# Performance work log

Measured on AMD Instinct MI355X. Metric: run time of the kernel, lower is better.

The kernel has to match this reference:

```python
import jax, jax.numpy as jnp
import numpy as np

N = 50000          # nodes
E_RAND = 800000    # random edges
E = E_RAND + N     # + self loops -> 850000
F_IN = 256         # nembed
F_HID = 64         # nhid
H = 8              # nheads
NCLASS = 40
ALPHA = 0.2        # leakyrelu slope


def setup_inputs() -> dict:
    key = jax.random.key(0)
    ks = jax.random.split(key, 8)
    x = jax.random.normal(ks[0], (N, F_IN), dtype=jnp.float32)
    # random edges + self loops (guarantees every row-sum > 0, like adj + I)
    er = jax.random.randint(ks[1], (2, E_RAND), 0, N, dtype=jnp.int32)
    loops = jnp.tile(jnp.arange(N, dtype=jnp.int32)[None, :], (2, 1))
    edge_index = jnp.concatenate([er, loops], axis=1)  # [2, E]
    # per-head attention params (xavier-ish scale)
    W = jax.random.normal(ks[2], (H, F_IN, F_HID), dtype=jnp.float32) * (1.0 / np.sqrt(F_IN))
    a = jax.random.normal(ks[3], (H, 2 * F_HID), dtype=jnp.float32) * 0.1
    Wo = jax.random.normal(ks[4], (H * F_HID, F_HID), dtype=jnp.float32) * (1.0 / np.sqrt(H * F_HID))
    ao = jax.random.normal(ks[5], (2 * F_HID,), dtype=jnp.float32) * 0.1
    mlp_w = jax.random.normal(ks[6], (NCLASS, F_HID), dtype=jnp.float32) * 0.05
    mlp_b = jnp.zeros((NCLASS,), dtype=jnp.float32)
    return {"x": x, "edge_index": edge_index, "W": W, "a": a,
            "Wo": Wo, "ao": ao, "mlp_w": mlp_w, "mlp_b": mlp_b}


def _leaky(v):
    return jnp.where(v > 0, v, ALPHA * v)


def _spgat_layer(x, W, a, src, dst, n):
    """pyGAT SpGraphAttentionLayer (eval mode, dropout = identity).
    out[i] = sum_{e: src=i} exp(-leakyrelu(a.[h_src;h_dst])) * h[dst] / rowsum_i
    """
    h = x @ W                         # [N, D]
    D = W.shape[1]
    s_src = h @ a[:D]                 # [N]
    s_dst = h @ a[D:]                 # [N]
    # per-edge unnormalized attention (note the -exp(leaky) of original sp impl)
    e = jnp.exp(-_leaky(s_src[src] + s_dst[dst]))          # [E]
    rowsum = jax.ops.segment_sum(e, src, num_segments=n)   # [N]
    num = jax.ops.segment_sum(e[:, None] * h[dst], src, num_segments=n)  # [N, D]
    return num / rowsum[:, None]


def reference(x, edge_index, W, a, Wo, ao, mlp_w, mlp_b):
    src, dst = edge_index[0], edge_index[1]
    # multi-head attention, concat=True -> elu inside each head
    heads = [jax.nn.elu(_spgat_layer(x, W[i], a[i], src, dst, N)) for i in range(H)]
    xc = jnp.concatenate(heads, axis=1)                     # [N, H*F_HID]
    # dropout (eval) = identity
    xo = jax.nn.elu(_spgat_layer(xc, Wo, ao, src, dst, N))  # [N, F_HID]
    return xo @ mlp_w.T + mlp_b                             # [N, NCLASS]
```

## Files before the change

### kernel.cpp

```cpp
#include <hip/hip_runtime.h>

#define NN 50000
#define HH 8
#define ALPHA 0.2f
#define NPAD 50048

typedef short short8 __attribute__((ext_vector_type(8)));
typedef float f32x4 __attribute__((ext_vector_type(4)));

__device__ __forceinline__ float elu_f(float x) {
  return x > 0.f ? x : __expf(x) - 1.f;
}

__device__ __forceinline__ unsigned short f2bf(float f) {
  unsigned int u = __float_as_uint(f);
  unsigned int r = (u + 0x7fffu + ((u >> 16) & 1u)) >> 16;
  return (unsigned short)r;
}

__global__ void cvt_x_kernel(const float* __restrict__ x, unsigned short* __restrict__ xb,
                             int total4) {
  int i = blockIdx.x * 256 + threadIdx.x;
  if (i >= total4) return;
  float4 v = ((const float4*)x)[i];
  ushort4 o;
  o.x = f2bf(v.x); o.y = f2bf(v.y); o.z = f2bf(v.z); o.w = f2bf(v.w);
  ((ushort4*)xb)[i] = o;
}

__global__ void cvt_w_kernel(const float* __restrict__ W, unsigned short* __restrict__ Wt,
                             int K, int total) {
  int tid = blockIdx.x * 256 + threadIdx.x;
  if (tid >= total) return;
  int h = tid / (K * 64);
  int rem = tid - h * K * 64;
  int k = rem >> 6, c = rem & 63;
  Wt[((size_t)h * 64 + c) * K + k] = f2bf(W[tid]);
}

__global__ void hist_kernel(const int* __restrict__ src, int* __restrict__ cnt, int E) {
  int e = blockIdx.x * blockDim.x + threadIdx.x;
  if (e < E) atomicAdd(&cnt[src[e]], 1);
}

__global__ __launch_bounds__(1024) void scan_blocks_kernel(const int* __restrict__ cnt,
    int* __restrict__ tmp, int* __restrict__ bsum, int n) {
  __shared__ int sh[1024];
  int i = blockIdx.x * 1024 + threadIdx.x;
  int v = (i < n) ? cnt[i] : 0;
  sh[threadIdx.x] = v;
  __syncthreads();
  for (int off = 1; off < 1024; off <<= 1) {
    int t = (threadIdx.x >= off) ? sh[threadIdx.x - off] : 0;
    __syncthreads();
    sh[threadIdx.x] += t;
    __syncthreads();
  }
  if (i < n) tmp[i] = sh[threadIdx.x] - v;
  if (threadIdx.x == 1023) bsum[blockIdx.x] = sh[1023];
}

__global__ __launch_bounds__(64) void scan_top_kernel(const int* __restrict__ bsum,
    int* __restrict__ boffs, int nb) {
  int L = threadIdx.x;
  int v = (L < nb) ? bsum[L] : 0;
  int incl = v;
#pragma unroll
  for (int off = 1; off < 64; off <<= 1) {
    int t = __shfl_up(incl, off, 64);
    if (L >= off) incl += t;
  }
  if (L < nb) boffs[L] = incl - v;
}

__global__ __launch_bounds__(1024) void scan_apply_kernel(const int* __restrict__ tmp,
    const int* __restrict__ boffs, int* __restrict__ row_ptr, int* __restrict__ nxt,
    int n, int E) {
  int i = blockIdx.x * 1024 + threadIdx.x;
  if (i < n) {
    int s = tmp[i] + boffs[blockIdx.x];
    row_ptr[i] = s;
    nxt[i] = s;
  }
  if (i == 0) row_ptr[n] = E;
}

__global__ void scatter_kernel(const int* __restrict__ src, const int* __restrict__ dst,
                               int* __restrict__ nxt, int* __restrict__ col, int E) {
  int e = blockIdx.x * blockDim.x + threadIdx.x;
  if (e < E) {
    int p = atomicAdd(&nxt[src[e]], 1);
    col[p] = dst[e];
  }
}

template <int MT>
__global__ __launch_bounds__(256) void mfma_gemm_kernel(
    const unsigned short* __restrict__ A, const unsigned short* __restrict__ Bt,
    const float* __restrict__ Aatt, unsigned short* __restrict__ Cout,
    float* __restrict__ ss, float* __restrict__ sd,
    int N, int K, int tab_stride, int score_stride) {
  extern __shared__ unsigned short Bs[];
  const int y = blockIdx.y;
  const int Kp = K + 8;

  {
    const unsigned short* Bsrc = Bt + (size_t)y * 64 * K;
    int nchunk = 64 * (K >> 3);
    for (int c = threadIdx.x; c < nchunk; c += 256) {
      int n = c / (K >> 3);
      int kq = (c - n * (K >> 3)) << 3;
      *(uint4*)&Bs[n * Kp + kq] = *(const uint4*)(Bsrc + (size_t)n * K + kq);
    }
  }
  __syncthreads();

  int w = threadIdx.x >> 6, L = threadIdx.x & 63;
  int quad = L >> 4, l16 = L & 15;
  int m0 = blockIdx.x * (64 * MT) + w * (16 * MT);

  f32x4 acc[MT][4];
#pragma unroll
  for (int mt = 0; mt < MT; ++mt)
#pragma unroll
    for (int nt = 0; nt < 4; ++nt) acc[mt][nt] = (f32x4)(0.f);

  const unsigned short* Arow[MT];
#pragma unroll
  for (int mt = 0; mt < MT; ++mt)
    Arow[mt] = A + (size_t)(m0 + mt * 16 + l16) * K + quad * 8;

  short8 a_cur[MT];
#pragma unroll
  for (int mt = 0; mt < MT; ++mt) a_cur[mt] = *(const short8*)(Arow[mt]);

  for (int k0 = 0; k0 < K; k0 += 32) {
    short8 a_nxt[MT];
    if (k0 + 32 < K) {
#pragma unroll
      for (int mt = 0; mt < MT; ++mt) a_nxt[mt] = *(const short8*)(Arow[mt] + k0 + 32);
    }
#pragma unroll
    for (int nt = 0; nt < 4; ++nt) {
      short8 b = *(const short8*)&Bs[(l16 + 16 * nt) * Kp + k0 + quad * 8];
#pragma unroll
      for (int mt = 0; mt < MT; ++mt)
        acc[mt][nt] = __builtin_amdgcn_mfma_f32_16x16x32_bf16(a_cur[mt], b, acc[mt][nt], 0, 0, 0);
    }
#pragma unroll
    for (int mt = 0; mt < MT; ++mt) a_cur[mt] = a_nxt[mt];
  }

  float as[4], ad[4];
#pragma unroll
  for (int nt = 0; nt < 4; ++nt) {
    as[nt] = Aatt[y * 128 + l16 + 16 * nt];
    ad[nt] = Aatt[y * 128 + 64 + l16 + 16 * nt];
  }
#pragma unroll
  for (int mt = 0; mt < MT; ++mt) {
#pragma unroll
    for (int reg = 0; reg < 4; ++reg) {
      float p = 0.f, q = 0.f;
#pragma unroll
      for (int nt = 0; nt < 4; ++nt) {
        p += acc[mt][nt][reg] * as[nt];
        q += acc[mt][nt][reg] * ad[nt];
      }
#pragma unroll
      for (int off = 1; off < 16; off <<= 1) {
        p += __shfl_xor(p, off, 64);
        q += __shfl_xor(q, off, 64);
      }
      int row = m0 + mt * 16 + quad * 4 + reg;
      if (l16 == 0 && row < N) {
        ss[(size_t)row * score_stride + y] = p;
        sd[(size_t)row * score_stride + y] = q;
      }
    }
#pragma unroll
    for (int reg = 0; reg < 4; ++reg) {
      int row = m0 + mt * 16 + quad * 4 + reg;
      if (row < N) {
#pragma unroll
        for (int nt = 0; nt < 4; ++nt)
          Cout[(size_t)row * tab_stride + y * 64 + l16 + 16 * nt] = f2bf(acc[mt][nt][reg]);
      }
    }
  }
}

__global__ __launch_bounds__(256) void agg1_kernel(const unsigned short* __restrict__ table,
    const float* __restrict__ ss, const float* __restrict__ sd,
    const int* __restrict__ row_ptr, const int* __restrict__ col,
    unsigned short* __restrict__ xc, int N) {
  int wid = threadIdx.x >> 6, L = threadIdx.x & 63;
  int n = blockIdx.x * 4 + wid;
  if (n >= N) return;
  int h = L >> 3;
  int b = L & 7;
  int srcsel = h << 3;
  float ssn = ss[n * 8 + h];
  int k0 = row_ptr[n], deg = row_ptr[n + 1] - k0;
  float acc[8];
#pragma unroll
  for (int t = 0; t < 8; ++t) acc[t] = 0.f;
  float rs = 0.f;

  for (int c0 = 0; c0 < deg; c0 += 64) {
    int j = c0 + L;
    int d_l = (j < deg) ? col[k0 + j] : 0;
    int m = min(64, deg - c0);
    for (int g = 0; g < m; g += 8) {
      int eoff = g + b;
      int de = __shfl(d_l, eoff, 64);
      float sv = sd[(size_t)de * 8 + h];
      float s = ssn + sv;
      float e = __expf(-fmaxf(s, ALPHA * s));
      if (eoff >= m) e = 0.f;
      rs += e;
      int gm = min(8, m - g);
      int d0 = __builtin_amdgcn_readlane(d_l, g);
      uint4 rv = *((const uint4*)(table + (size_t)d0 * 512) + L);
      for (int jj = 0; jj < gm; ++jj) {
        uint4 cur = rv;
        if (jj + 1 < gm) {
          int dn = __builtin_amdgcn_readlane(d_l, g + jj + 1);
          rv = *((const uint4*)(table + (size_t)dn * 512) + L);
        }
        float ew = __shfl(e, srcsel + jj, 64);
        const unsigned int* up = (const unsigned int*)&cur;
#pragma unroll
        for (int w = 0; w < 4; ++w) {
          acc[2 * w]     += ew * __uint_as_float(up[w] << 16);
          acc[2 * w + 1] += ew * __uint_as_float(up[w] & 0xffff0000u);
        }
      }
    }
  }
  rs += __shfl_xor(rs, 1, 64);
  rs += __shfl_xor(rs, 2, 64);
  rs += __shfl_xor(rs, 4, 64);
  float inv = 1.f / rs;
  short8 pk;
#pragma unroll
  for (int t = 0; t < 8; ++t) pk[t] = (short)f2bf(elu_f(acc[t] * inv));
  *(short8*)(xc + (size_t)n * 512 + L * 8) = pk;
}

__global__ __launch_bounds__(256) void agg2_kernel(const unsigned short* __restrict__ table,
    const float* __restrict__ ss, const float* __restrict__ sd,
    const int* __restrict__ row_ptr, const int* __restrict__ col,
    float* __restrict__ xo, int N) {
  int wid = threadIdx.x >> 6, L = threadIdx.x & 63;
  int n = blockIdx.x * 4 + wid;
  if (n >= N) return;
  float ssn = ss[n];
  int k0 = row_ptr[n], deg = row_ptr[n + 1] - k0;
  float acc = 0.f, rs = 0.f;
  const char* base = (const char*)table;

  for (int c0 = 0; c0 < deg; c0 += 64) {
    int j = c0 + L;
    int d_l = 0;
    float e_l = 0.f;
    if (j < deg) {
      d_l = col[k0 + j];
      float s = ssn + sd[d_l];
      e_l = __expf(-fmaxf(s, ALPHA * s));
    }
    rs += e_l;
    int m = min(64, deg - c0);
    int off_l = d_l << 7;
    int so = __builtin_amdgcn_readlane(off_l, 0);
    unsigned hv = *(const unsigned short*)(base + so + L * 2);
    for (int jj = 0; jj < m; ++jj) {
      unsigned cur = hv;
      if (jj + 1 < m) {
        so = __builtin_amdgcn_readlane(off_l, jj + 1);
        hv = *(const unsigned short*)(base + so + L * 2);
      }
      float ew = __uint_as_float(
          (unsigned)__builtin_amdgcn_readlane(__float_as_uint(e_l), jj));
      acc += ew * __uint_as_float(cur << 16);
    }
  }
#pragma unroll
  for (int off = 1; off < 64; off <<= 1) rs += __shfl_xor(rs, off, 64);
  xo[(size_t)n * 64 + L] = elu_f(acc / rs);
}

__global__ __launch_bounds__(256) void final_kernel(const float* __restrict__ xo,
    const float* __restrict__ mlp_w, const float* __restrict__ mlp_b,
    float* __restrict__ out, int total) {
  __shared__ float wsh[40 * 65];
  __shared__ float bsh[40];
  for (int i = threadIdx.x; i < 40 * 64; i += 256) wsh[(i >> 6) * 65 + (i & 63)] = mlp_w[i];
  if (threadIdx.x < 40) bsh[threadIdx.x] = mlp_b[threadIdx.x];
  __syncthreads();
  int idx = blockIdx.x * 256 + threadIdx.x;
  if (idx >= total) return;
  int n = idx / 40, c = idx - n * 40;
  const float* xr = xo + (size_t)n * 64;
  const float* wr = wsh + c * 65;
  float acc = bsh[c];
#pragma unroll
  for (int j = 0; j < 64; ++j) acc += xr[j] * wr[j];
  out[idx] = acc;
}

extern "C" void kernel_launch(void* const* d_in, const int* in_sizes, int n_in,
                              void* d_out, int out_size, void* d_ws, size_t ws_size,
                              hipStream_t stream) {
  (void)n_in; (void)out_size; (void)ws_size;
  const float* x  = (const float*)d_in[0];
  const int*   ei = (const int*)d_in[1];
  const float* W  = (const float*)d_in[2];
  const float* a  = (const float*)d_in[3];
  const float* Wo = (const float*)d_in[4];
  const float* ao = (const float*)d_in[5];
  const float* mw = (const float*)d_in[6];
  const float* mb = (const float*)d_in[7];
  float* out = (float*)d_out;

  const int N = NN;
  const int E = in_sizes[1] / 2;
  const int* src = ei;
  const int* dst = ei + E;

  char* ws = (char*)d_ws;
  size_t off = 0;
  auto alloc = [&](size_t bytes) {
    char* p = ws + off;
    off = (off + bytes + 255) & ~(size_t)255;
    return p;
  };
  unsigned short* xb  = (unsigned short*)alloc((size_t)NPAD * 256 * 2);
  unsigned short* Wt  = (unsigned short*)alloc((size_t)HH * 64 * 256 * 2);
  unsigned short* Wot = (unsigned short*)alloc((size_t)64 * 512 * 2);
  unsigned short* h1b = (unsigned short*)alloc((size_t)N * 512 * 2);
  float* ss1     = (float*)alloc((size_t)N * 8 * 4);
  float* sd1     = (float*)alloc((size_t)N * 8 * 4);
  unsigned short* xc = (unsigned short*)alloc((size_t)NPAD * 512 * 2);
  unsigned short* h2b = (unsigned short*)alloc((size_t)N * 64 * 2);
  float* ss2     = (float*)alloc((size_t)N * 4);
  float* sd2     = (float*)alloc((size_t)N * 4);
  float* xo      = (float*)alloc((size_t)N * 64 * 4);
  int*   row_ptr = (int*)  alloc((size_t)(N + 1) * 4);
  int*   nxt     = (int*)  alloc((size_t)N * 4);
  int*   cnt     = (int*)  alloc((size_t)N * 4);
  int*   tmp     = (int*)  alloc((size_t)N * 4);
  int*   bsum    = (int*)  alloc(64 * 4);
  int*   boffs   = (int*)  alloc(64 * 4);
  int*   colv    = (int*)  alloc((size_t)E * 4);

  int eb = (E + 255) / 256;
  int nb1024 = (N + 1023) / 1024;

  hipLaunchKernelGGL(cvt_x_kernel, dim3((N * 256 / 4 + 255) / 256), dim3(256), 0, stream,
                     x, xb, N * 256 / 4);
  hipLaunchKernelGGL(cvt_w_kernel, dim3((HH * 256 * 64 + 255) / 256), dim3(256), 0, stream,
                     W, Wt, 256, HH * 256 * 64);
  hipLaunchKernelGGL(cvt_w_kernel, dim3((512 * 64 + 255) / 256), dim3(256), 0, stream,
                     Wo, Wot, 512, 512 * 64);

  hipMemsetAsync(cnt, 0, (size_t)N * 4, stream);
  hipLaunchKernelGGL(hist_kernel, dim3(eb), dim3(256), 0, stream, src, cnt, E);
  hipLaunchKernelGGL(scan_blocks_kernel, dim3(nb1024), dim3(1024), 0, stream, cnt, tmp, bsum, N);
  hipLaunchKernelGGL(scan_top_kernel, dim3(1), dim3(64), 0, stream, bsum, boffs, nb1024);
  hipLaunchKernelGGL(scan_apply_kernel, dim3(nb1024), dim3(1024), 0, stream, tmp, boffs, row_ptr, nxt, N, E);
  hipLaunchKernelGGL(scatter_kernel, dim3(eb), dim3(256), 0, stream, src, dst, nxt, colv, E);

  hipLaunchKernelGGL((mfma_gemm_kernel<2>), dim3(NPAD / 128, HH), dim3(256),
                     64 * (256 + 8) * 2, stream,
                     xb, Wt, a, h1b, ss1, sd1, N, 256, 512, 8);
  hipLaunchKernelGGL(agg1_kernel, dim3((N + 3) / 4), dim3(256), 0, stream,
                     h1b, ss1, sd1, row_ptr, colv, xc, N);

  hipLaunchKernelGGL((mfma_gemm_kernel<1>), dim3(NPAD / 64, 1), dim3(256),
                     64 * (512 + 8) * 2, stream,
                     xc, Wot, ao, h2b, ss2, sd2, N, 512, 64, 1);
  hipLaunchKernelGGL(agg2_kernel, dim3((N + 3) / 4), dim3(256), 0, stream,
                     h2b, ss2, sd2, row_ptr, colv, xo, N);

  hipLaunchKernelGGL(final_kernel, dim3((N * 40 + 255) / 256), dim3(256), 0, stream,
                     xo, mw, mb, out, N * 40);
}
```

Baseline: 494.1 us.

## Fuse conversion kernels, restructure GEMM1 over heads, batch gather loads in aggregation

Merges the three fp32-to-bf16 conversion kernels into one launch. The first GEMM now loads each block's A rows into registers once and loops over all 8 heads, reloading B per head, instead of using a 2D grid that re-reads A for every head. Both aggregation kernels issue up to 8 independent gather loads before consuming them, replacing the one-ahead software prefetch, to raise memory-level parallelism. This costs more registers and adds per-head syncthreads in the GEMM, and the GEMM launches fewer, longer blocks.

```diff
diff --git a/kernel.cpp b/kernel.cpp
--- a/kernel.cpp
+++ b/kernel.cpp
@@ -18,24 +18,31 @@
   return (unsigned short)r;
 }
 
-__global__ void cvt_x_kernel(const float* __restrict__ x, unsigned short* __restrict__ xb,
-                             int total4) {
-  int i = blockIdx.x * 256 + threadIdx.x;
-  if (i >= total4) return;
-  float4 v = ((const float4*)x)[i];
-  ushort4 o;
-  o.x = f2bf(v.x); o.y = f2bf(v.y); o.z = f2bf(v.z); o.w = f2bf(v.w);
-  ((ushort4*)xb)[i] = o;
-}
-
-__global__ void cvt_w_kernel(const float* __restrict__ W, unsigned short* __restrict__ Wt,
-                             int K, int total) {
+__global__ void cvt_all_kernel(const float* __restrict__ x, unsigned short* __restrict__ xb,
+                               const float* __restrict__ W, unsigned short* __restrict__ Wt,
+                               const float* __restrict__ Wo, unsigned short* __restrict__ Wot,
+                               int n4x) {
   int tid = blockIdx.x * 256 + threadIdx.x;
-  if (tid >= total) return;
-  int h = tid / (K * 64);
-  int rem = tid - h * K * 64;
-  int k = rem >> 6, c = rem & 63;
-  Wt[((size_t)h * 64 + c) * K + k] = f2bf(W[tid]);
+  if (tid < n4x) {
+    float4 v = ((const float4*)x)[tid];
+    ushort4 o;
+    o.x = f2bf(v.x); o.y = f2bf(v.y); o.z = f2bf(v.z); o.w = f2bf(v.w);
+    ((ushort4*)xb)[tid] = o;
+    return;
+  }
+  int t1 = tid - n4x;
+  if (t1 < HH * 256 * 64) {
+    int h = t1 / (256 * 64);
+    int rem = t1 - h * 256 * 64;
+    int k = rem >> 6, c = rem & 63;
+    Wt[((size_t)h * 64 + c) * 256 + k] = f2bf(W[t1]);
+    return;
+  }
+  int t2 = t1 - HH * 256 * 64;
+  if (t2 < 512 * 64) {
+    int k = t2 >> 6, c = t2 & 63;
+    Wot[(size_t)c * 512 + k] = f2bf(Wo[t2]);
+  }
 }
 
 __global__ void hist_kernel(const int* __restrict__ src, int* __restrict__ cnt, int E) {
@@ -94,98 +101,147 @@
   }
 }
 
-template <int MT>
-__global__ __launch_bounds__(256) void mfma_gemm_kernel(
+__global__ __launch_bounds__(256) void mfma_gemm1_kernel(
     const unsigned short* __restrict__ A, const unsigned short* __restrict__ Bt,
     const float* __restrict__ Aatt, unsigned short* __restrict__ Cout,
-    float* __restrict__ ss, float* __restrict__ sd,
-    int N, int K, int tab_stride, int score_stride) {
-  extern __shared__ unsigned short Bs[];
-  const int y = blockIdx.y;
-  const int Kp = K + 8;
-
-  {
-    const unsigned short* Bsrc = Bt + (size_t)y * 64 * K;
-    int nchunk = 64 * (K >> 3);
-    for (int c = threadIdx.x; c < nchunk; c += 256) {
-      int n = c / (K >> 3);
-      int kq = (c - n * (K >> 3)) << 3;
-      *(uint4*)&Bs[n * Kp + kq] = *(const uint4*)(Bsrc + (size_t)n * K + kq);
-    }
-  }
-  __syncthreads();
-
+    float* __restrict__ ss, float* __restrict__ sd, int N) {
+  __shared__ unsigned short Bs[64][264];
   int w = threadIdx.x >> 6, L = threadIdx.x & 63;
   int quad = L >> 4, l16 = L & 15;
-  int m0 = blockIdx.x * (64 * MT) + w * (16 * MT);
-
-  f32x4 acc[MT][4];
-#pragma unroll
-  for (int mt = 0; mt < MT; ++mt)
-#pragma unroll
-    for (int nt = 0; nt < 4; ++nt) acc[mt][nt] = (f32x4)(0.f);
-
-  const unsigned short* Arow[MT];
-#pragma unroll
-  for (int mt = 0; mt < MT; ++mt)
-    Arow[mt] = A + (size_t)(m0 + mt * 16 + l16) * K + quad * 8;
-
-  short8 a_cur[MT];
-#pragma unroll
-  for (int mt = 0; mt < MT; ++mt) a_cur[mt] = *(const short8*)(Arow[mt]);
-
-  for (int k0 = 0; k0 < K; k0 += 32) {
-    short8 a_nxt[MT];
-    if (k0 + 32 < K) {
-#pragma unroll
-      for (int mt = 0; mt < MT; ++mt) a_nxt[mt] = *(const short8*)(Arow[mt] + k0 + 32);
-    }
+  int m0 = blockIdx.x * 64;
+  int myrow = m0 + w * 16 + l16;
+
+  const unsigned short* Ar = A + (size_t)myrow * 256 + quad * 8;
+  short8 areg[8];
+#pragma unroll
+  for (int ks = 0; ks < 8; ++ks) areg[ks] = *(const short8*)(Ar + ks * 32);
+
+  for (int y = 0; y < HH; ++y) {
+    __syncthreads();
+    {
+      const unsigned short* Bsrc = Bt + (size_t)y * 64 * 256;
+      for (int c = threadIdx.x; c < 2048; c += 256) {
+        int n = c >> 5;
+        int kq = (c & 31) << 3;
+        *(uint4*)&Bs[n][kq] = *(const uint4*)(Bsrc + (size_t)n * 256 + kq);
+      }
+    }
+    __syncthreads();
+
+    f32x4 acc[4];
+#pragma unroll
+    for (int nt = 0; nt < 4; ++nt) acc[nt] = (f32x4)(0.f);
+#pragma unroll
+    for (int ks = 0; ks < 8; ++ks) {
+#pragma unroll
+      for (int nt = 0; nt < 4; ++nt) {
+        short8 b = *(const short8*)&Bs[l16 + 16 * nt][ks * 32 + quad * 8];
+        acc[nt] = __builtin_amdgcn_mfma_f32_16x16x32_bf16(areg[ks], b, acc[nt], 0, 0, 0);
+      }
+    }
+
+    float as[4], ad[4];
 #pragma unroll
     for (int nt = 0; nt < 4; ++nt) {
-      short8 b = *(const short8*)&Bs[(l16 + 16 * nt) * Kp + k0 + quad * 8];
-#pragma unroll
-      for (int mt = 0; mt < MT; ++mt)
-        acc[mt][nt] = __builtin_amdgcn_mfma_f32_16x16x32_bf16(a_cur[mt], b, acc[mt][nt], 0, 0, 0);
-    }
-#pragma unroll
-    for (int mt = 0; mt < MT; ++mt) a_cur[mt] = a_nxt[mt];
-  }
-
-  float as[4], ad[4];
-#pragma unroll
-  for (int nt = 0; nt < 4; ++nt) {
-    as[nt] = Aatt[y * 128 + l16 + 16 * nt];
-    ad[nt] = Aatt[y * 128 + 64 + l16 + 16 * nt];
-  }
-#pragma unroll
-  for (int mt = 0; mt < MT; ++mt) {
+      as[nt] = Aatt[y * 128 + l16 + 16 * nt];
+      ad[nt] = Aatt[y * 128 + 64 + l16 + 16 * nt];
+    }
 #pragma unroll
     for (int reg = 0; reg < 4; ++reg) {
       float p = 0.f, q = 0.f;
 #pragma unroll
       for (int nt = 0; nt < 4; ++nt) {
-        p += acc[mt][nt][reg] * as[nt];
-        q += acc[mt][nt][reg] * ad[nt];
+        p += acc[nt][reg] * as[nt];
+        q += acc[nt][reg] * ad[nt];
       }
 #pragma unroll
       for (int off = 1; off < 16; off <<= 1) {
         p += __shfl_xor(p, off, 64);
         q += __shfl_xor(q, off, 64);
       }
-      int row = m0 + mt * 16 + quad * 4 + reg;
+      int row = m0 + w * 16 + quad * 4 + reg;
       if (l16 == 0 && row < N) {
-        ss[(size_t)row * score_stride + y] = p;
-        sd[(size_t)row * score_stride + y] = q;
+        ss[(size_t)row * 8 + y] = p;
+        sd[(size_t)row * 8 + y] = q;
       }
     }
 #pragma unroll
     for (int reg = 0; reg < 4; ++reg) {
-      int row = m0 + mt * 16 + quad * 4 + reg;
+      int row = m0 + w * 16 + quad * 4 + reg;
       if (row < N) {
 #pragma unroll
         for (int nt = 0; nt < 4; ++nt)
-          Cout[(size_t)row * tab_stride + y * 64 + l16 + 16 * nt] = f2bf(acc[mt][nt][reg]);
-      }
+          Cout[(size_t)row * 512 + y * 64 + l16 + 16 * nt] = f2bf(acc[nt][reg]);
+      }
+    }
+  }
+}
+
+__global__ __launch_bounds__(256) void mfma_gemm2_kernel(
+    const unsigned short* __restrict__ A, const unsigned short* __restrict__ Bt,
+    const float* __restrict__ Aatt, unsigned short* __restrict__ Cout,
+    float* __restrict__ ss, float* __restrict__ sd, int N) {
+  __shared__ unsigned short Bs[64][520];
+  {
+    for (int c = threadIdx.x; c < 4096; c += 256) {
+      int n = c >> 6;
+      int kq = (c & 63) << 3;
+      *(uint4*)&Bs[n][kq] = *(const uint4*)(Bt + (size_t)n * 512 + kq);
+    }
+  }
+  __syncthreads();
+
+  int w = threadIdx.x >> 6, L = threadIdx.x & 63;
+  int quad = L >> 4, l16 = L & 15;
+  int m0 = blockIdx.x * 64;
+  int myrow = m0 + w * 16 + l16;
+  const unsigned short* Ar = A + (size_t)myrow * 512 + quad * 8;
+
+  f32x4 acc[4];
+#pragma unroll
+  for (int nt = 0; nt < 4; ++nt) acc[nt] = (f32x4)(0.f);
+
+  short8 a_cur = *(const short8*)(Ar);
+  for (int k0 = 0; k0 < 512; k0 += 32) {
+    short8 a_nxt;
+    if (k0 + 32 < 512) a_nxt = *(const short8*)(Ar + k0 + 32);
+#pragma unroll
+    for (int nt = 0; nt < 4; ++nt) {
+      short8 b = *(const short8*)&Bs[l16 + 16 * nt][k0 + quad * 8];
+      acc[nt] = __builtin_amdgcn_mfma_f32_16x16x32_bf16(a_cur, b, acc[nt], 0, 0, 0);
+    }
+    a_cur = a_nxt;
+  }
+
+  float as[4], ad[4];
+#pragma unroll
+  for (int nt = 0; nt < 4; ++nt) {
+    as[nt] = Aatt[l16 + 16 * nt];
+    ad[nt] = Aatt[64 + l16 + 16 * nt];
+  }
+#pragma unroll
+  for (int reg = 0; reg < 4; ++reg) {
+    float p = 0.f, q = 0.f;
+#pragma unroll
+    for (int nt = 0; nt < 4; ++nt) {
+      p += acc[nt][reg] * as[nt];
+      q += acc[nt][reg] * ad[nt];
+    }
+#pragma unroll
+    for (int off = 1; off < 16; off <<= 1) {
+      p += __shfl_xor(p, off, 64);
+      q += __shfl_xor(q, off, 64);
+    }
+    int row = m0 + w * 16 + quad * 4 + reg;
+    if (l16 == 0 && row < N) { ss[row] = p; sd[row] = q; }
+  }
+#pragma unroll
+  for (int reg = 0; reg < 4; ++reg) {
+    int row = m0 + w * 16 + quad * 4 + reg;
+    if (row < N) {
+#pragma unroll
+      for (int nt = 0; nt < 4; ++nt)
+        Cout[(size_t)row * 64 + l16 + 16 * nt] = f2bf(acc[nt][reg]);
     }
   }
 }
@@ -214,26 +270,29 @@
     for (int g = 0; g < m; g += 8) {
       int eoff = g + b;
       int de = __shfl(d_l, eoff, 64);
-      float sv = sd[(size_t)de * 8 + h];
-      float s = ssn + sv;
+      float s = ssn + sd[(size_t)de * 8 + h];
       float e = __expf(-fmaxf(s, ALPHA * s));
       if (eoff >= m) e = 0.f;
       rs += e;
       int gm = min(8, m - g);
-      int d0 = __builtin_amdgcn_readlane(d_l, g);
-      uint4 rv = *((const uint4*)(table + (size_t)d0 * 512) + L);
-      for (int jj = 0; jj < gm; ++jj) {
-        uint4 cur = rv;
-        if (jj + 1 < gm) {
-          int dn = __builtin_amdgcn_readlane(d_l, g + jj + 1);
-          rv = *((const uint4*)(table + (size_t)dn * 512) + L);
+      uint4 rv[8];
+#pragma unroll
+      for (int t = 0; t < 8; ++t) {
+        if (t < gm) {
+          int dg = __builtin_amdgcn_readlane(d_l, g + t);
+          rv[t] = *((const uint4*)(table + (size_t)dg * 512) + L);
         }
-        float ew = __shfl(e, srcsel + jj, 64);
-        const unsigned int* up = (const unsigned int*)&cur;
-#pragma unroll
-        for (int w = 0; w < 4; ++w) {
-          acc[2 * w]     += ew * __uint_as_float(up[w] << 16);
-          acc[2 * w + 1] += ew * __uint_as_float(up[w] & 0xffff0000u);
+      }
+#pragma unroll
+      for (int t = 0; t < 8; ++t) {
+        if (t < gm) {
+          float ew = __shfl(e, srcsel + t, 64);
+          const unsigned int* up = (const unsigned int*)&rv[t];
+#pragma unroll
+          for (int v = 0; v < 4; ++v) {
+            acc[2 * v]     += ew * __uint_as_float(up[v] << 16);
+            acc[2 * v + 1] += ew * __uint_as_float(up[v] & 0xffff0000u);
+          }
         }
       }
     }
@@ -272,17 +331,24 @@
     rs += e_l;
     int m = min(64, deg - c0);
     int off_l = d_l << 7;
-    int so = __builtin_amdgcn_readlane(off_l, 0);
-    unsigned hv = *(const unsigned short*)(base + so + L * 2);
-    for (int jj = 0; jj < m; ++jj) {
-      unsigned cur = hv;
-      if (jj + 1 < m) {
-        so = __builtin_amdgcn_readlane(off_l, jj + 1);
-        hv = *(const unsigned short*)(base + so + L * 2);
-      }
-      float ew = __uint_as_float(
-          (unsigned)__builtin_amdgcn_readlane(__float_as_uint(e_l), jj));
-      acc += ew * __uint_as_float(cur << 16);
+    for (int g = 0; g < m; g += 8) {
+      int gm = min(8, m - g);
+      unsigned hv[8];
+#pragma unroll
+      for (int t = 0; t < 8; ++t) {
+        if (t < gm) {
+          int so = __builtin_amdgcn_readlane(off_l, g + t);
+          hv[t] = *(const unsigned short*)(base + so + L * 2);
+        }
+      }
+#pragma unroll
+      for (int t = 0; t < 8; ++t) {
+        if (t < gm) {
+          float ew = __uint_as_float(
+              (unsigned)__builtin_amdgcn_readlane(__float_as_uint(e_l), g + t));
+          acc += ew * __uint_as_float(hv[t] << 16);
+        }
+      }
     }
   }
 #pragma unroll
@@ -356,13 +422,11 @@
 
   int eb = (E + 255) / 256;
   int nb1024 = (N + 1023) / 1024;
-
-  hipLaunchKernelGGL(cvt_x_kernel, dim3((N * 256 / 4 + 255) / 256), dim3(256), 0, stream,
-                     x, xb, N * 256 / 4);
-  hipLaunchKernelGGL(cvt_w_kernel, dim3((HH * 256 * 64 + 255) / 256), dim3(256), 0, stream,
-                     W, Wt, 256, HH * 256 * 64);
-  hipLaunchKernelGGL(cvt_w_kernel, dim3((512 * 64 + 255) / 256), dim3(256), 0, stream,
-                     Wo, Wot, 512, 512 * 64);
+  int n4x = N * 256 / 4;
+  int cvt_total = n4x + HH * 256 * 64 + 512 * 64;
+
+  hipLaunchKernelGGL(cvt_all_kernel, dim3((cvt_total + 255) / 256), dim3(256), 0, stream,
+                     x, xb, W, Wt, Wo, Wot, n4x);
 
   hipMemsetAsync(cnt, 0, (size_t)N * 4, stream);
   hipLaunchKernelGGL(hist_kernel, dim3(eb), dim3(256), 0, stream, src, cnt, E);
@@ -371,15 +435,13 @@
   hipLaunchKernelGGL(scan_apply_kernel, dim3(nb1024), dim3(1024), 0, stream, tmp, boffs, row_ptr, nxt, N, E);
   hipLaunchKernelGGL(scatter_kernel, dim3(eb), dim3(256), 0, stream, src, dst, nxt, colv, E);
 
-  hipLaunchKernelGGL((mfma_gemm_kernel<2>), dim3(NPAD / 128, HH), dim3(256),
-                     64 * (256 + 8) * 2, stream,
-                     xb, Wt, a, h1b, ss1, sd1, N, 256, 512, 8);
+  hipLaunchKernelGGL(mfma_gemm1_kernel, dim3(NPAD / 64), dim3(256), 0, stream,
+                     xb, Wt, a, h1b, ss1, sd1, N);
   hipLaunchKernelGGL(agg1_kernel, dim3((N + 3) / 4), dim3(256), 0, stream,
                      h1b, ss1, sd1, row_ptr, colv, xc, N);
 
-  hipLaunchKernelGGL((mfma_gemm_kernel<1>), dim3(NPAD / 64, 1), dim3(256),
-                     64 * (512 + 8) * 2, stream,
-                     xc, Wot, ao, h2b, ss2, sd2, N, 512, 64, 1);
+  hipLaunchKernelGGL(mfma_gemm2_kernel, dim3(NPAD / 64), dim3(256), 0, stream,
+                     xc, Wot, ao, h2b, ss2, sd2, N);
   hipLaunchKernelGGL(agg2_kernel, dim3((N + 3) / 4), dim3(256), 0, stream,
                      h2b, ss2, sd2, row_ptr, colv, xo, N);
 
```

New measurement: 457.2 us. 1.08x faster.
